# Kernel optimization log

Measured on AMD Instinct MI355X. Metric: run time of the kernel, lower is better.

## Reference

```python
import jax, jax.numpy as jnp
import numpy as np

C = 512          # channels
NH = 8           # num_heads
ENC = 512        # encoder_channels
SCALE_P = 1.0    # channels_scale_for_positional_embedding
CP = int(C * SCALE_P)
GROUPS = 32


def group_norm(x, g, b, eps=1e-5):
    # x: (N, C, L); GroupNorm32 computes stats in fp32
    N, Ch, L = x.shape
    xg = x.reshape(N, GROUPS, Ch // GROUPS, L).astype(jnp.float32)
    mu = xg.mean(axis=(2, 3), keepdims=True)
    var = xg.var(axis=(2, 3), keepdims=True)
    xn = ((xg - mu) * jax.lax.rsqrt(var + eps)).reshape(N, Ch, L).astype(x.dtype)
    return xn * g[None, :, None] + b[None, :, None]


def conv1(x, W, b):
    # 1x1 conv1d: x (N, Cin, L), W (Cout, Cin), b (Cout)
    return jnp.einsum('oc,ncl->nol', W, x) + b[None, :, None]


def setup_inputs() -> dict:
    key = jax.random.key(0)
    ks = iter(jax.random.split(key, 40))
    rn = lambda *s: jax.random.normal(next(ks), s, dtype=jnp.float32)
    inp = {
        'x': rn(8, C, 32, 32),
        'xf_out': rn(8, ENC, 64),
        'obj_contour_embedding': rn(8, ENC, 64),
        'obj_description_embedding': rn(8, ENC, 64),
        'image_patch_contour_embedding': rn(8, ENC, 1024),
        # norm_for_qkv
        'gn_qkv_g': jnp.ones(C), 'gn_qkv_b': jnp.zeros(C),
        # projectors (1x1 conv weights); zero_module proj_out given random weights for a meaningful baseline
        'W_self_qkv': rn(3 * C, C) * 0.02, 'b_self_qkv': jnp.zeros(3 * C),
        'W_cross_q': rn(C, C) * 0.02, 'b_cross_q': jnp.zeros(C),
        'W_content': rn(2 * C, ENC) * 0.02, 'b_content': jnp.zeros(2 * C),
        'W_pos': rn(CP, ENC) * 0.02, 'b_pos': jnp.zeros(CP),
        'gn_desc_g': jnp.ones(ENC), 'gn_desc_b': jnp.zeros(ENC),
        'gn_cpos_g': jnp.ones(CP), 'gn_cpos_b': jnp.zeros(CP),
        'gn_ipos_g': jnp.ones(CP), 'gn_ipos_b': jnp.zeros(CP),
        'W_self_out': rn(C, C) * 0.02, 'b_self_out': jnp.zeros(C),
        'W_cross_out': rn(C, C) * 0.02, 'b_cross_out': jnp.zeros(C),
    }
    return inp


def _attn(q, k, v, scale):
    # q,k: (B, Cq, T/S), v: (B, Cv, S)
    w = jnp.einsum('bct,bcs->bts', q * scale, k * scale)
    w = jax.nn.softmax(w.astype(jnp.float32), axis=-1).astype(q.dtype)
    return jnp.einsum('bts,bcs->bct', w, v)


def reference(x, xf_out, obj_contour_embedding, obj_description_embedding,
              image_patch_contour_embedding,
              gn_qkv_g, gn_qkv_b, W_self_qkv, b_self_qkv, W_cross_q, b_cross_q,
              W_content, b_content, W_pos, b_pos,
              gn_desc_g, gn_desc_b, gn_cpos_g, gn_cpos_b, gn_ipos_g, gn_ipos_b,
              W_self_out, b_self_out, W_cross_out, b_cross_out):
    b_, c_, h_, w_ = x.shape
    xf = x.reshape(b_, c_, -1)                      # (N, C, L1)
    L1 = xf.shape[-1]
    L2 = obj_contour_embedding.shape[-1]
    dc = C // NH
    dp = CP // NH
    scale = float(int((1 + SCALE_P) * C) // NH) ** -0.25

    # ---- self-attention over image patches ----
    qkv = conv1(group_norm(xf, gn_qkv_g, gn_qkv_b), W_self_qkv, b_self_qkv)
    sq, sk, sv = jnp.split(qkv, 3, axis=1)
    sq = sq.reshape(b_ * NH, dc, L1)
    sk = sk.reshape(b_ * NH, dc, L1)
    sv = sv.reshape(b_ * NH, dc, L1)

    ipos = conv1(image_patch_contour_embedding, W_pos, b_pos)
    ipos = group_norm(ipos, gn_ipos_g, gn_ipos_b)
    ipos = ipos.reshape(b_ * NH, dp, L1)

    sq = jnp.concatenate([sq, ipos], axis=1)
    sk = jnp.concatenate([sk, ipos], axis=1)
    self_out = _attn(sq, sk, sv, scale).reshape(b_, C, L1)
    self_out = conv1(self_out, W_self_out, b_self_out)
    xf = xf + self_out

    # ---- cross-attention to object tokens ----
    cq = conv1(group_norm(xf, gn_qkv_g, gn_qkv_b), W_cross_q, b_cross_q)
    cq = cq.reshape(b_ * NH, dc, L1)
    cq = jnp.concatenate([cq, ipos], axis=1)

    cpos = conv1(obj_contour_embedding, W_pos, b_pos)
    cpos = group_norm(cpos, gn_cpos_g, gn_cpos_b)
    cpos = cpos.reshape(b_ * NH, dp, L2)

    content = (xf_out + group_norm(obj_description_embedding, gn_desc_g, gn_desc_b)) / 2
    kv = conv1(content, W_content, b_content)
    ck, cv = jnp.split(kv, 2, axis=1)
    ck = ck.reshape(b_ * NH, dc, L2)
    cv = cv.reshape(b_ * NH, dc, L2)
    ck = jnp.concatenate([ck, cpos], axis=1)

    cross_out = _attn(cq, ck, cv, scale).reshape(b_, C, L1)
    cross_out = conv1(cross_out, W_cross_out, b_cross_out)

    return (xf + cross_out).reshape(b_, c_, h_, w_)
```

## Files before the change

kernel.cpp:

```cpp
#include <hip/hip_runtime.h>

typedef unsigned short u16;
typedef __attribute__((ext_vector_type(8))) short bf16x8;
typedef __attribute__((ext_vector_type(4))) float f32x4;

__device__ __forceinline__ float bf2f(u16 u) {
  union { unsigned int i; float f; } v;
  v.i = ((unsigned int)u) << 16;
  return v.f;
}
__device__ __forceinline__ u16 f2bf(float f) {
  union { float f; unsigned int i; } v;
  v.f = f;
  unsigned int r = v.i + 0x7FFFu + ((v.i >> 16) & 1u);
  return (u16)(r >> 16);
}
__device__ __forceinline__ unsigned int cvtpk(float lo, float hi) {
  unsigned int r;
  asm("v_cvt_pk_bf16_f32 %0, %1, %2" : "=v"(r) : "v"(lo), "v"(hi));
  return r;
}

__device__ __forceinline__ float4 ld4f(const float* p) {
  return *reinterpret_cast<const float4*>(p);
}
__device__ __forceinline__ float4 ld4f(const u16* p) {
  uint2 v = *reinterpret_cast<const uint2*>(p);
  float4 r;
  r.x = bf2f((u16)(v.x & 0xffff)); r.y = bf2f((u16)(v.x >> 16));
  r.z = bf2f((u16)(v.y & 0xffff)); r.w = bf2f((u16)(v.y >> 16));
  return r;
}

template <typename TIN>
__global__ __launch_bounds__(1024) void gn_kernel(
    const TIN* __restrict__ In, u16* __restrict__ OutBuf,
    const float* __restrict__ G, const float* __restrict__ Bt,
    const float* __restrict__ Add, float post_scale,
    int C, int L, int cpg)
{
  const int blk = blockIdx.x;
  const int n = blk >> 5, grp = blk & 31;
  const size_t base = ((size_t)n * C + (size_t)grp * cpg) * L;
  const int cnt = cpg * L;
  const int cnt4 = cnt >> 2;
  const int tid = threadIdx.x;

  float s = 0.f, s2 = 0.f;
  for (int i = tid; i < cnt4; i += 1024) {
    float4 v = ld4f(In + base + (size_t)i * 4);
    s += v.x + v.y + v.z + v.w;
    s2 += v.x * v.x + v.y * v.y + v.z * v.z + v.w * v.w;
  }
#pragma unroll
  for (int d = 1; d < 64; d <<= 1) {
    s += __shfl_xor(s, d);
    s2 += __shfl_xor(s2, d);
  }
  __shared__ float ps[16], ps2[16], stat[2];
  const int wid = tid >> 6;
  if ((tid & 63) == 0) { ps[wid] = s; ps2[wid] = s2; }
  __syncthreads();
  if (tid == 0) {
    float a = 0.f, b2 = 0.f;
#pragma unroll
    for (int w = 0; w < 16; ++w) { a += ps[w]; b2 += ps2[w]; }
    const float mean = a / cnt;
    const float var = b2 / cnt - mean * mean;
    stat[0] = mean;
    stat[1] = rsqrtf(var + 1e-5f);
  }
  __syncthreads();
  const float mean = stat[0], rstd = stat[1];

  for (int i = tid; i < cnt4; i += 1024) {
    const int i4 = i * 4;
    const int ch = grp * cpg + i4 / L;
    float4 v = ld4f(In + base + i4);
    const float g = G[ch] * rstd, bt = Bt[ch] - mean * rstd * G[ch];
    float4 r;
    r.x = v.x * g + bt; r.y = v.y * g + bt;
    r.z = v.z * g + bt; r.w = v.w * g + bt;
    if (Add) {
      float4 a = *reinterpret_cast<const float4*>(Add + base + i4);
      r.x = (r.x + a.x) * post_scale; r.y = (r.y + a.y) * post_scale;
      r.z = (r.z + a.z) * post_scale; r.w = (r.w + a.w) * post_scale;
    }
    uint2 o;
    o.x = (unsigned int)f2bf(r.x) | ((unsigned int)f2bf(r.y) << 16);
    o.y = (unsigned int)f2bf(r.z) | ((unsigned int)f2bf(r.w) << 16);
    *reinterpret_cast<uint2*>(OutBuf + base + i4) = o;
  }
}

__device__ __forceinline__ void loadpair4(const u16* p0, const u16* p1,
                                          unsigned int* bw) {
  uint2 a = *reinterpret_cast<const uint2*>(p0);
  uint2 c = *reinterpret_cast<const uint2*>(p1);
  bw[0] = (a.x & 0xffffu) | (c.x << 16);
  bw[1] = (a.x >> 16) | (c.x & 0xffff0000u);
  bw[2] = (a.y & 0xffffu) | (c.y << 16);
  bw[3] = (a.y >> 16) | (c.y & 0xffff0000u);
}
__device__ __forceinline__ void loadpair4(const float* p0, const float* p1,
                                          unsigned int* bw) {
  float4 a = *reinterpret_cast<const float4*>(p0);
  float4 c = *reinterpret_cast<const float4*>(p1);
  bw[0] = cvtpk(a.x, c.x); bw[1] = cvtpk(a.y, c.y);
  bw[2] = cvtpk(a.z, c.z); bw[3] = cvtpk(a.w, c.w);
}

template <typename TX, int LT>
__global__ __launch_bounds__(256) void gemm_conv(
    const TX* __restrict__ X, const float* __restrict__ W,
    const float* __restrict__ Bias,
    u16* __restrict__ OutBf, float* __restrict__ Out32,
    const float* __restrict__ Res,
    int Cin, int L, int O, int mode)
{
  constexpr int NL = LT / 16;
  __shared__ __align__(16) u16 As[64][40];
  __shared__ __align__(16) u16 Bs[LT][40];
  const int tid = threadIdx.x;
  const int wave = tid >> 6;
  const int lane = tid & 63;
  const int n = blockIdx.z;
  const int o0 = blockIdx.x * 64;
  const int l0 = blockIdx.y * LT;
  const TX* Xn = X + (size_t)n * Cin * L;

  const int ao = tid >> 2, akc = (tid & 3) * 8;
  const int c2 = (tid & 15) * 2, lt0 = (tid >> 4) * NL;
  const float* wp = W + (size_t)(o0 + ao) * Cin + akc;
  const TX* xp0 = Xn + (size_t)c2 * L + l0 + lt0;
  const TX* xp1 = xp0 + L;

  f32x4 acc[NL];
#pragma unroll
  for (int i = 0; i < NL; ++i) acc[i] = (f32x4){0.f, 0.f, 0.f, 0.f};

  const int row = lane & 15;
  const int kh = (lane >> 4) * 8;

  float4 wa = *reinterpret_cast<const float4*>(wp);
  float4 wb = *reinterpret_cast<const float4*>(wp + 4);
  unsigned int bw[NL];
#pragma unroll
  for (int ch = 0; ch < NL; ch += 4)
    loadpair4(xp0 + ch, xp1 + ch, bw + ch);

  const int nK = Cin >> 5;
  for (int kt = 0; kt < nK; ++kt) {
    {
      uint4 ap;
      ap.x = cvtpk(wa.x, wa.y); ap.y = cvtpk(wa.z, wa.w);
      ap.z = cvtpk(wb.x, wb.y); ap.w = cvtpk(wb.z, wb.w);
      *reinterpret_cast<uint4*>(&As[ao][akc]) = ap;
    }
#pragma unroll
    for (int j = 0; j < NL; ++j)
      *reinterpret_cast<unsigned int*>(&Bs[lt0 + j][c2]) = bw[j];
    __syncthreads();

    if (kt + 1 < nK) {
      const int k0 = (kt + 1) * 32;
      wa = *reinterpret_cast<const float4*>(wp + k0);
      wb = *reinterpret_cast<const float4*>(wp + k0 + 4);
#pragma unroll
      for (int ch = 0; ch < NL; ch += 4)
        loadpair4(xp0 + (size_t)k0 * L + ch, xp1 + (size_t)k0 * L + ch, bw + ch);
    }

    bf16x8 a = *reinterpret_cast<const bf16x8*>(&As[wave * 16 + row][kh]);
#pragma unroll
    for (int lt = 0; lt < NL; ++lt) {
      bf16x8 b = *reinterpret_cast<const bf16x8*>(&Bs[lt * 16 + row][kh]);
      acc[lt] = __builtin_amdgcn_mfma_f32_16x16x32_bf16(a, b, acc[lt], 0, 0, 0);
    }
    __syncthreads();
  }

  const int col = lane & 15;
  const int r0 = (lane >> 4) * 4;
#pragma unroll
  for (int lt = 0; lt < NL; ++lt) {
    const int ll = l0 + lt * 16 + col;
#pragma unroll
    for (int j = 0; j < 4; ++j) {
      const int oo = o0 + wave * 16 + r0 + j;
      float v = acc[lt][j] + Bias[oo];
      const size_t idx = ((size_t)n * O + oo) * L + ll;
      if (mode == 1) {
        Out32[idx] = v + Res[idx];
      } else {
        OutBf[idx] = f2bf(v);
      }
    }
  }
}

__global__ __launch_bounds__(256, 2) void flash_attn(
    const u16* __restrict__ qA, int qA_C, int qA_off,
    const u16* __restrict__ qB,
    const u16* __restrict__ kA, int kA_C, int kA_off,
    const u16* __restrict__ kB,
    const u16* __restrict__ V, int v_C, int v_off,
    u16* __restrict__ Out, int S_len, float qscale)
{
  __shared__ __align__(16) u16 smem[32768];
  u16* const Qs = smem;
  u16* const K0 = smem;
  u16* const K1 = smem + 8192;
  u16* const Ps = smem + 16384;
  u16* const V0 = smem + 24576;
  u16* const V1 = smem + 28672;

  const int tid = threadIdx.x;
  const int wave = tid >> 6, lane = tid & 63;
  const int b = blockIdx.y >> 3, h = blockIdx.y & 7;
  const int t0 = blockIdx.x * 128;
  const int l16 = lane & 15, q4 = lane >> 4;
  const int swz = (l16 & 7) << 3;

  const int c2 = (tid & 63) * 2;
  const u16* q0 = (c2 < 64)
      ? qA + ((size_t)b * qA_C + qA_off + h * 64 + c2) * 1024 + t0
      : qB + ((size_t)b * 512 + h * 64 + (c2 - 64)) * 1024 + t0;
  const u16* q1 = q0 + 1024;
  const u16* k0 = (c2 < 64)
      ? kA + ((size_t)b * kA_C + kA_off + h * 64 + c2) * (size_t)S_len
      : kB + ((size_t)b * 512 + h * 64 + (c2 - 64)) * (size_t)S_len;
  const u16* k1 = k0 + S_len;
  const u16* vb = V + ((size_t)b * v_C + v_off + h * 64) * (size_t)S_len;

  const int s8 = (tid >> 6) * 8;
  const int cv0 = tid >> 3, sb0 = (tid & 7) * 8;
  const int cv1 = (tid + 256) >> 3, sb1 = sb0;

  uint4 kr0a = *reinterpret_cast<const uint4*>(k0 + s8);
  uint4 kr0c = *reinterpret_cast<const uint4*>(k1 + s8);
  uint4 kr1a = *reinterpret_cast<const uint4*>(k0 + s8 + 32);
  uint4 kr1c = *reinterpret_cast<const uint4*>(k1 + s8 + 32);
  uint4 vr0 = *reinterpret_cast<const uint4*>(vb + (size_t)cv0 * S_len + sb0);
  uint4 vr1 = *reinterpret_cast<const uint4*>(vb + (size_t)cv1 * S_len + sb1);

#pragma unroll
  for (int it = 0; it < 4; ++it) {
    const int t8 = (tid >> 6) * 8 + it * 32;
    union { uint4 q; u16 u[8]; } a, c;
    a.q = *reinterpret_cast<const uint4*>(q0 + t8);
    c.q = *reinterpret_cast<const uint4*>(q1 + t8);
#pragma unroll
    for (int j = 0; j < 8; ++j) {
      const unsigned int w =
          cvtpk(bf2f(a.u[j]) * qscale, bf2f(c.u[j]) * qscale);
      *reinterpret_cast<unsigned int*>(&Qs[(t8 + j) * 128 + (c2 ^ (j << 3))]) = w;
    }
  }
  __syncthreads();

  bf16x8 qf[2][4];
#pragma unroll
  for (int g = 0; g < 2; ++g)
#pragma unroll
    for (int kk = 0; kk < 4; ++kk)
      qf[g][kk] = *reinterpret_cast<const bf16x8*>(
          &Qs[(wave * 32 + g * 16 + l16) * 128 + ((kk * 32 + q4 * 8) ^ swz)]);
  __syncthreads();

  auto writeK = [&](u16* Kd) {
    union { uint4 q; u16 u[8]; } a, c;
    a.q = kr0a; c.q = kr0c;
#pragma unroll
    for (int j = 0; j < 8; ++j)
      *reinterpret_cast<unsigned int*>(&Kd[(s8 + j) * 128 + (c2 ^ (j << 3))]) =
          (unsigned int)a.u[j] | ((unsigned int)c.u[j] << 16);
    a.q = kr1a; c.q = kr1c;
#pragma unroll
    for (int j = 0; j < 8; ++j)
      *reinterpret_cast<unsigned int*>(&Kd[(s8 + 32 + j) * 128 + (c2 ^ (j << 3))]) =
          (unsigned int)a.u[j] | ((unsigned int)c.u[j] << 16);
  };
  auto writeV = [&](u16* Vd) {
    *reinterpret_cast<uint4*>(&Vd[cv0 * 64 + (sb0 ^ ((cv0 & 7) << 3))]) = vr0;
    *reinterpret_cast<uint4*>(&Vd[cv1 * 64 + (sb1 ^ ((cv1 & 7) << 3))]) = vr1;
  };

  writeK(K0);
  writeV(V0);
  __syncthreads();

  float m_run[2][4], l_run[2][4];
  f32x4 o_acc[2][4];
#pragma unroll
  for (int g = 0; g < 2; ++g)
#pragma unroll
    for (int j = 0; j < 4; ++j) {
      m_run[g][j] = -1e30f; l_run[g][j] = 0.f;
      o_acc[g][j] = (f32x4){0.f, 0.f, 0.f, 0.f};
    }

  const int NT = S_len >> 6;
  int p = 0;
  for (int t = 0; t < NT; ++t) {
    u16* const Kp = p ? K1 : K0;
    u16* const Vp = p ? V1 : V0;

    if (t + 1 < NT) {
      const int sc = (t + 1) * 64;
      kr0a = *reinterpret_cast<const uint4*>(k0 + sc + s8);
      kr0c = *reinterpret_cast<const uint4*>(k1 + sc + s8);
      kr1a = *reinterpret_cast<const uint4*>(k0 + sc + s8 + 32);
      kr1c = *reinterpret_cast<const uint4*>(k1 + sc + s8 + 32);
      vr0 = *reinterpret_cast<const uint4*>(vb + (size_t)cv0 * S_len + sc + sb0);
      vr1 = *reinterpret_cast<const uint4*>(vb + (size_t)cv1 * S_len + sc + sb1);
    }

    f32x4 sacc[2][4];
#pragma unroll
    for (int g = 0; g < 2; ++g)
#pragma unroll
      for (int st = 0; st < 4; ++st) sacc[g][st] = (f32x4){0.f, 0.f, 0.f, 0.f};
    __builtin_amdgcn_s_setprio(1);
#pragma unroll
    for (int st = 0; st < 4; ++st) {
#pragma unroll
      for (int kk = 0; kk < 4; ++kk) {
        bf16x8 kf = *reinterpret_cast<const bf16x8*>(
            &Kp[(st * 16 + l16) * 128 + ((kk * 32 + q4 * 8) ^ swz)]);
        sacc[0][st] = __builtin_amdgcn_mfma_f32_16x16x32_bf16(qf[0][kk], kf, sacc[0][st], 0, 0, 0);
        sacc[1][st] = __builtin_amdgcn_mfma_f32_16x16x32_bf16(qf[1][kk], kf, sacc[1][st], 0, 0, 0);
      }
    }
    __builtin_amdgcn_s_setprio(0);

#pragma unroll
    for (int g = 0; g < 2; ++g) {
      float mt[4];
#pragma unroll
      for (int j = 0; j < 4; ++j)
        mt[j] = fmaxf(fmaxf(sacc[g][0][j], sacc[g][1][j]),
                      fmaxf(sacc[g][2][j], sacc[g][3][j]));
#pragma unroll
      for (int d = 1; d < 16; d <<= 1)
#pragma unroll
        for (int j = 0; j < 4; ++j) mt[j] = fmaxf(mt[j], __shfl_xor(mt[j], d));

      float corr[4], ls[4];
#pragma unroll
      for (int j = 0; j < 4; ++j) {
        const float mn = fmaxf(m_run[g][j], mt[j]);
        corr[j] = exp2f(m_run[g][j] - mn);
        m_run[g][j] = mn;
        ls[j] = 0.f;
      }
      float pv[4][4];
#pragma unroll
      for (int st = 0; st < 4; ++st)
#pragma unroll
        for (int j = 0; j < 4; ++j) {
          pv[st][j] = exp2f(sacc[g][st][j] - m_run[g][j]);
          ls[j] += pv[st][j];
        }
#pragma unroll
      for (int d = 1; d < 16; d <<= 1)
#pragma unroll
        for (int j = 0; j < 4; ++j) ls[j] += __shfl_xor(ls[j], d);
#pragma unroll
      for (int j = 0; j < 4; ++j) l_run[g][j] = l_run[g][j] * corr[j] + ls[j];

#pragma unroll
      for (int st = 0; st < 4; ++st)
#pragma unroll
        for (int j2 = 0; j2 < 2; ++j2) {
          const unsigned int pk = cvtpk(pv[st][2 * j2], pv[st][2 * j2 + 1]);
          const int r0 = wave * 32 + g * 16 + q4 * 4 + 2 * j2;
          Ps[r0 * 64 + ((st * 16 + l16) ^ ((r0 & 7) << 3))] = (u16)pk;
          const int r1 = r0 + 1;
          Ps[r1 * 64 + ((st * 16 + l16) ^ ((r1 & 7) << 3))] = (u16)(pk >> 16);
        }

#pragma unroll
      for (int ct = 0; ct < 4; ++ct)
#pragma unroll
        for (int j = 0; j < 4; ++j) o_acc[g][ct][j] *= corr[j];
    }

    bf16x8 pa[2][2];
#pragma unroll
    for (int g = 0; g < 2; ++g)
#pragma unroll
      for (int ks = 0; ks < 2; ++ks)
        pa[g][ks] = *reinterpret_cast<const bf16x8*>(
            &Ps[(wave * 32 + g * 16 + l16) * 64 + ((ks * 32 + q4 * 8) ^ swz)]);
    __builtin_amdgcn_s_setprio(1);
#pragma unroll
    for (int ct = 0; ct < 4; ++ct) {
#pragma unroll
      for (int ks = 0; ks < 2; ++ks) {
        bf16x8 vf = *reinterpret_cast<const bf16x8*>(
            &Vp[(ct * 16 + l16) * 64 + ((ks * 32 + q4 * 8) ^ swz)]);
        o_acc[0][ct] = __builtin_amdgcn_mfma_f32_16x16x32_bf16(pa[0][ks], vf, o_acc[0][ct], 0, 0, 0);
        o_acc[1][ct] = __builtin_amdgcn_mfma_f32_16x16x32_bf16(pa[1][ks], vf, o_acc[1][ct], 0, 0, 0);
      }
    }
    __builtin_amdgcn_s_setprio(0);

    if (t + 1 < NT) {
      writeK(p ? K0 : K1);
      writeV(p ? V0 : V1);
    }
    __syncthreads();
    p ^= 1;
  }

#pragma unroll
  for (int g = 0; g < 2; ++g) {
    float inv[4];
#pragma unroll
    for (int j = 0; j < 4; ++j) inv[j] = 1.f / l_run[g][j];
    const size_t obase =
        ((size_t)b * 512 + h * 64) * 1024 + t0 + wave * 32 + g * 16 + q4 * 4;
#pragma unroll
    for (int ct = 0; ct < 4; ++ct) {
      const unsigned int p0 = cvtpk(o_acc[g][ct][0] * inv[0], o_acc[g][ct][1] * inv[1]);
      const unsigned int p1 = cvtpk(o_acc[g][ct][2] * inv[2], o_acc[g][ct][3] * inv[3]);
      const unsigned long long d =
          (unsigned long long)p0 | ((unsigned long long)p1 << 32);
      *reinterpret_cast<unsigned long long*>(
          Out + obase + (size_t)(ct * 16 + l16) * 1024) = d;
    }
  }
}

extern "C" void kernel_launch(void* const* d_in, const int* in_sizes, int n_in,
                              void* d_out, int out_size, void* d_ws, size_t ws_size,
                              hipStream_t stream) {
  const float* X_in        = (const float*)d_in[0];
  const float* xf_out      = (const float*)d_in[1];
  const float* obj_cont    = (const float*)d_in[2];
  const float* obj_desc    = (const float*)d_in[3];
  const float* ipce        = (const float*)d_in[4];
  const float* gn_qkv_g    = (const float*)d_in[5];
  const float* gn_qkv_b    = (const float*)d_in[6];
  const float* W_self_qkv  = (const float*)d_in[7];
  const float* b_self_qkv  = (const float*)d_in[8];
  const float* W_cross_q   = (const float*)d_in[9];
  const float* b_cross_q   = (const float*)d_in[10];
  const float* W_content   = (const float*)d_in[11];
  const float* b_content   = (const float*)d_in[12];
  const float* W_pos       = (const float*)d_in[13];
  const float* b_pos       = (const float*)d_in[14];
  const float* gn_desc_g   = (const float*)d_in[15];
  const float* gn_desc_b   = (const float*)d_in[16];
  const float* gn_cpos_g   = (const float*)d_in[17];
  const float* gn_cpos_b   = (const float*)d_in[18];
  const float* gn_ipos_g   = (const float*)d_in[19];
  const float* gn_ipos_b   = (const float*)d_in[20];
  const float* W_self_out  = (const float*)d_in[21];
  const float* b_self_out  = (const float*)d_in[22];
  const float* W_cross_out = (const float*)d_in[23];
  const float* b_cross_out = (const float*)d_in[24];

  char* base = (char*)d_ws;
  u16* A = (u16*)base;
  u16* B = (u16*)(base + 8 * 1024 * 1024);
  u16* C = (u16*)(base + 32 * 1024 * 1024);
  u16* D = (u16*)(base + 40 * 1024 * 1024);

  u16* norm1 = A;
  u16* norm2 = A;
  u16* cposr   = A;
  u16* cpos    = A + 262144;
  u16* content = A + 2 * 262144;
  u16* kvbuf   = A + 3 * 262144;
  u16* qkv  = B;
  u16* cq   = B;
  u16* ipos = C;
  u16* iposr = D;
  u16* attn1 = D;
  u16* cattn = D;
  float* xf32 = (float*)d_out;
  float* outp = (float*)d_out;

  const float qscale = 0.08838834764831845f * 1.4426950408889634f;
  dim3 blk(256);
  dim3 blkgn(1024);

  gn_kernel<float><<<dim3(256), blkgn, 0, stream>>>(X_in, norm1, gn_qkv_g, gn_qkv_b,
                                                    nullptr, 1.f, 512, 1024, 16);
  gemm_conv<u16, 128><<<dim3(24, 8, 8), blk, 0, stream>>>(norm1, W_self_qkv, b_self_qkv,
                                                          qkv, nullptr, nullptr,
                                                          512, 1024, 1536, 0);
  gemm_conv<float, 128><<<dim3(8, 8, 8), blk, 0, stream>>>(ipce, W_pos, b_pos, iposr,
                                                           nullptr, nullptr,
                                                           512, 1024, 512, 0);
  gn_kernel<u16><<<dim3(256), blkgn, 0, stream>>>(iposr, ipos, gn_ipos_g, gn_ipos_b,
                                                  nullptr, 1.f, 512, 1024, 16);
  flash_attn<<<dim3(8, 64), blk, 0, stream>>>(qkv, 1536, 0, ipos,
                                              qkv, 1536, 512, ipos,
                                              qkv, 1536, 1024,
                                              attn1, 1024, qscale);
  gemm_conv<u16, 128><<<dim3(8, 8, 8), blk, 0, stream>>>(attn1, W_self_out, b_self_out,
                                                         nullptr, xf32, X_in,
                                                         512, 1024, 512, 1);
  gn_kernel<float><<<dim3(256), blkgn, 0, stream>>>(xf32, norm2, gn_qkv_g, gn_qkv_b,
                                                    nullptr, 1.f, 512, 1024, 16);
  gemm_conv<u16, 128><<<dim3(8, 8, 8), blk, 0, stream>>>(norm2, W_cross_q, b_cross_q, cq,
                                                         nullptr, nullptr,
                                                         512, 1024, 512, 0);
  gemm_conv<float, 64><<<dim3(8, 1, 8), blk, 0, stream>>>(obj_cont, W_pos, b_pos, cposr,
                                                          nullptr, nullptr,
                                                          512, 64, 512, 0);
  gn_kernel<u16><<<dim3(256), blkgn, 0, stream>>>(cposr, cpos, gn_cpos_g, gn_cpos_b,
                                                  nullptr, 1.f, 512, 64, 16);
  gn_kernel<float><<<dim3(256), blkgn, 0, stream>>>(obj_desc, content, gn_desc_g,
                                                    gn_desc_b, xf_out, 0.5f, 512, 64, 16);
  gemm_conv<u16, 64><<<dim3(16, 1, 8), blk, 0, stream>>>(content, W_content, b_content,
                                                         kvbuf, nullptr, nullptr,
                                                         512, 64, 1024, 0);
  flash_attn<<<dim3(8, 64), blk, 0, stream>>>(cq, 512, 0, ipos,
                                              kvbuf, 1024, 0, cpos,
                                              kvbuf, 1024, 512,
                                              cattn, 64, qscale);
  gemm_conv<u16, 128><<<dim3(8, 8, 8), blk, 0, stream>>>(cattn, W_cross_out, b_cross_out,
                                                         nullptr, outp, xf32,
                                                         512, 1024, 512, 1);
}
```

Measured before the change: 295.8 us.

## Use 128x128 GEMM tiles with 512 threads and single-buffer attention K/V

The large 1x1-conv GEMMs move from 64x128 tiles with 256 threads to 128x128 tiles with 512 threads (8 waves), so each block covers more output channels and reuses each staged input tile more. Small-L GEMMs get their own 64x64 kernel. Flash attention drops K/V double buffering to a single LDS buffer that is written at the top of each iteration, which cuts shared memory use but serialises loads against compute. The P and output packing also switch from v_cvt_pk_bf16 to per-element software rounding.

```diff
diff --git a/kernel.cpp b/kernel.cpp
--- a/kernel.cpp
+++ b/kernel.cpp
@@ -110,44 +110,40 @@
   bw[2] = cvtpk(a.z, c.z); bw[3] = cvtpk(a.w, c.w);
 }
 
-template <typename TX, int LT>
-__global__ __launch_bounds__(256) void gemm_conv(
+template <typename TX>
+__global__ __launch_bounds__(256) void gemm_small(
     const TX* __restrict__ X, const float* __restrict__ W,
     const float* __restrict__ Bias,
-    u16* __restrict__ OutBf, float* __restrict__ Out32,
-    const float* __restrict__ Res,
-    int Cin, int L, int O, int mode)
+    u16* __restrict__ OutBf,
+    int Cin, int L, int O)
 {
-  constexpr int NL = LT / 16;
   __shared__ __align__(16) u16 As[64][40];
-  __shared__ __align__(16) u16 Bs[LT][40];
+  __shared__ __align__(16) u16 Bs[64][40];
   const int tid = threadIdx.x;
   const int wave = tid >> 6;
   const int lane = tid & 63;
   const int n = blockIdx.z;
   const int o0 = blockIdx.x * 64;
-  const int l0 = blockIdx.y * LT;
+  const int l0 = blockIdx.y * 64;
   const TX* Xn = X + (size_t)n * Cin * L;
 
   const int ao = tid >> 2, akc = (tid & 3) * 8;
-  const int c2 = (tid & 15) * 2, lt0 = (tid >> 4) * NL;
+  const int c2 = (tid & 15) * 2, lt0 = (tid >> 4) * 4;
   const float* wp = W + (size_t)(o0 + ao) * Cin + akc;
   const TX* xp0 = Xn + (size_t)c2 * L + l0 + lt0;
   const TX* xp1 = xp0 + L;
 
-  f32x4 acc[NL];
-#pragma unroll
-  for (int i = 0; i < NL; ++i) acc[i] = (f32x4){0.f, 0.f, 0.f, 0.f};
+  f32x4 acc[4];
+#pragma unroll
+  for (int i = 0; i < 4; ++i) acc[i] = (f32x4){0.f, 0.f, 0.f, 0.f};
 
   const int row = lane & 15;
   const int kh = (lane >> 4) * 8;
 
   float4 wa = *reinterpret_cast<const float4*>(wp);
   float4 wb = *reinterpret_cast<const float4*>(wp + 4);
-  unsigned int bw[NL];
-#pragma unroll
-  for (int ch = 0; ch < NL; ch += 4)
-    loadpair4(xp0 + ch, xp1 + ch, bw + ch);
+  unsigned int bw[4];
+  loadpair4(xp0, xp1, bw);
 
   const int nK = Cin >> 5;
   for (int kt = 0; kt < nK; ++kt) {
@@ -158,7 +154,7 @@
       *reinterpret_cast<uint4*>(&As[ao][akc]) = ap;
     }
 #pragma unroll
-    for (int j = 0; j < NL; ++j)
+    for (int j = 0; j < 4; ++j)
       *reinterpret_cast<unsigned int*>(&Bs[lt0 + j][c2]) = bw[j];
     __syncthreads();
 
@@ -166,14 +162,12 @@
       const int k0 = (kt + 1) * 32;
       wa = *reinterpret_cast<const float4*>(wp + k0);
       wb = *reinterpret_cast<const float4*>(wp + k0 + 4);
-#pragma unroll
-      for (int ch = 0; ch < NL; ch += 4)
-        loadpair4(xp0 + (size_t)k0 * L + ch, xp1 + (size_t)k0 * L + ch, bw + ch);
+      loadpair4(xp0 + (size_t)k0 * L, xp1 + (size_t)k0 * L, bw);
     }
 
     bf16x8 a = *reinterpret_cast<const bf16x8*>(&As[wave * 16 + row][kh]);
 #pragma unroll
-    for (int lt = 0; lt < NL; ++lt) {
+    for (int lt = 0; lt < 4; ++lt) {
       bf16x8 b = *reinterpret_cast<const bf16x8*>(&Bs[lt * 16 + row][kh]);
       acc[lt] = __builtin_amdgcn_mfma_f32_16x16x32_bf16(a, b, acc[lt], 0, 0, 0);
     }
@@ -183,7 +177,86 @@
   const int col = lane & 15;
   const int r0 = (lane >> 4) * 4;
 #pragma unroll
-  for (int lt = 0; lt < NL; ++lt) {
+  for (int lt = 0; lt < 4; ++lt) {
+    const int ll = l0 + lt * 16 + col;
+#pragma unroll
+    for (int j = 0; j < 4; ++j) {
+      const int oo = o0 + wave * 16 + r0 + j;
+      float v = acc[lt][j] + Bias[oo];
+      OutBf[((size_t)n * O + oo) * L + ll] = f2bf(v);
+    }
+  }
+}
+
+template <typename TX>
+__global__ __launch_bounds__(512) void gemm_big(
+    const TX* __restrict__ X, const float* __restrict__ W,
+    const float* __restrict__ Bias,
+    u16* __restrict__ OutBf, float* __restrict__ Out32,
+    const float* __restrict__ Res,
+    int Cin, int L, int O, int mode)
+{
+  __shared__ __align__(16) u16 As[128][40];
+  __shared__ __align__(16) u16 Bs[128][40];
+  const int tid = threadIdx.x;
+  const int wave = tid >> 6;
+  const int lane = tid & 63;
+  const int n = blockIdx.z;
+  const int o0 = blockIdx.x * 128;
+  const int l0 = blockIdx.y * 128;
+  const TX* Xn = X + (size_t)n * Cin * L;
+
+  const int ao = tid >> 2, akc = (tid & 3) * 8;
+  const int c2 = (tid & 15) * 2, lt0 = (tid >> 4) * 4;
+  const float* wp = W + (size_t)(o0 + ao) * Cin + akc;
+  const TX* xp0 = Xn + (size_t)c2 * L + l0 + lt0;
+  const TX* xp1 = xp0 + L;
+
+  f32x4 acc[8];
+#pragma unroll
+  for (int i = 0; i < 8; ++i) acc[i] = (f32x4){0.f, 0.f, 0.f, 0.f};
+
+  const int row = lane & 15;
+  const int kh = (lane >> 4) * 8;
+
+  float4 wa = *reinterpret_cast<const float4*>(wp);
+  float4 wb = *reinterpret_cast<const float4*>(wp + 4);
+  unsigned int bw[4];
+  loadpair4(xp0, xp1, bw);
+
+  const int nK = Cin >> 5;
+  for (int kt = 0; kt < nK; ++kt) {
+    {
+      uint4 ap;
+      ap.x = cvtpk(wa.x, wa.y); ap.y = cvtpk(wa.z, wa.w);
+      ap.z = cvtpk(wb.x, wb.y); ap.w = cvtpk(wb.z, wb.w);
+      *reinterpret_cast<uint4*>(&As[ao][akc]) = ap;
+    }
+#pragma unroll
+    for (int j = 0; j < 4; ++j)
+      *reinterpret_cast<unsigned int*>(&Bs[lt0 + j][c2]) = bw[j];
+    __syncthreads();
+
+    if (kt + 1 < nK) {
+      const int k0 = (kt + 1) * 32;
+      wa = *reinterpret_cast<const float4*>(wp + k0);
+      wb = *reinterpret_cast<const float4*>(wp + k0 + 4);
+      loadpair4(xp0 + (size_t)k0 * L, xp1 + (size_t)k0 * L, bw);
+    }
+
+    bf16x8 a = *reinterpret_cast<const bf16x8*>(&As[wave * 16 + row][kh]);
+#pragma unroll
+    for (int lt = 0; lt < 8; ++lt) {
+      bf16x8 b = *reinterpret_cast<const bf16x8*>(&Bs[lt * 16 + row][kh]);
+      acc[lt] = __builtin_amdgcn_mfma_f32_16x16x32_bf16(a, b, acc[lt], 0, 0, 0);
+    }
+    __syncthreads();
+  }
+
+  const int col = lane & 15;
+  const int r0 = (lane >> 4) * 4;
+#pragma unroll
+  for (int lt = 0; lt < 8; ++lt) {
     const int ll = l0 + lt * 16 + col;
 #pragma unroll
     for (int j = 0; j < 4; ++j) {
@@ -207,13 +280,11 @@
     const u16* __restrict__ V, int v_C, int v_off,
     u16* __restrict__ Out, int S_len, float qscale)
 {
-  __shared__ __align__(16) u16 smem[32768];
+  __shared__ __align__(16) u16 smem[20480];
   u16* const Qs = smem;
-  u16* const K0 = smem;
-  u16* const K1 = smem + 8192;
-  u16* const Ps = smem + 16384;
-  u16* const V0 = smem + 24576;
-  u16* const V1 = smem + 28672;
+  u16* const Ks = smem;
+  u16* const Ps = smem + 8192;
+  u16* const Vt = smem + 16384;
 
   const int tid = threadIdx.x;
   const int wave = tid >> 6, lane = tid & 63;
@@ -268,28 +339,6 @@
           &Qs[(wave * 32 + g * 16 + l16) * 128 + ((kk * 32 + q4 * 8) ^ swz)]);
   __syncthreads();
 
-  auto writeK = [&](u16* Kd) {
-    union { uint4 q; u16 u[8]; } a, c;
-    a.q = kr0a; c.q = kr0c;
-#pragma unroll
-    for (int j = 0; j < 8; ++j)
-      *reinterpret_cast<unsigned int*>(&Kd[(s8 + j) * 128 + (c2 ^ (j << 3))]) =
-          (unsigned int)a.u[j] | ((unsigned int)c.u[j] << 16);
-    a.q = kr1a; c.q = kr1c;
-#pragma unroll
-    for (int j = 0; j < 8; ++j)
-      *reinterpret_cast<unsigned int*>(&Kd[(s8 + 32 + j) * 128 + (c2 ^ (j << 3))]) =
-          (unsigned int)a.u[j] | ((unsigned int)c.u[j] << 16);
-  };
-  auto writeV = [&](u16* Vd) {
-    *reinterpret_cast<uint4*>(&Vd[cv0 * 64 + (sb0 ^ ((cv0 & 7) << 3))]) = vr0;
-    *reinterpret_cast<uint4*>(&Vd[cv1 * 64 + (sb1 ^ ((cv1 & 7) << 3))]) = vr1;
-  };
-
-  writeK(K0);
-  writeV(V0);
-  __syncthreads();
-
   float m_run[2][4], l_run[2][4];
   f32x4 o_acc[2][4];
 #pragma unroll
@@ -301,10 +350,23 @@
     }
 
   const int NT = S_len >> 6;
-  int p = 0;
   for (int t = 0; t < NT; ++t) {
-    u16* const Kp = p ? K1 : K0;
-    u16* const Vp = p ? V1 : V0;
+    {
+      union { uint4 q; u16 u[8]; } a, c;
+      a.q = kr0a; c.q = kr0c;
+#pragma unroll
+      for (int j = 0; j < 8; ++j)
+        *reinterpret_cast<unsigned int*>(&Ks[(s8 + j) * 128 + (c2 ^ (j << 3))]) =
+            (unsigned int)a.u[j] | ((unsigned int)c.u[j] << 16);
+      a.q = kr1a; c.q = kr1c;
+#pragma unroll
+      for (int j = 0; j < 8; ++j)
+        *reinterpret_cast<unsigned int*>(&Ks[(s8 + 32 + j) * 128 + (c2 ^ (j << 3))]) =
+            (unsigned int)a.u[j] | ((unsigned int)c.u[j] << 16);
+    }
+    *reinterpret_cast<uint4*>(&Vt[cv0 * 64 + (sb0 ^ ((cv0 & 7) << 3))]) = vr0;
+    *reinterpret_cast<uint4*>(&Vt[cv1 * 64 + (sb1 ^ ((cv1 & 7) << 3))]) = vr1;
+    __syncthreads();
 
     if (t + 1 < NT) {
       const int sc = (t + 1) * 64;
@@ -327,7 +389,7 @@
 #pragma unroll
       for (int kk = 0; kk < 4; ++kk) {
         bf16x8 kf = *reinterpret_cast<const bf16x8*>(
-            &Kp[(st * 16 + l16) * 128 + ((kk * 32 + q4 * 8) ^ swz)]);
+            &Ks[(st * 16 + l16) * 128 + ((kk * 32 + q4 * 8) ^ swz)]);
         sacc[0][st] = __builtin_amdgcn_mfma_f32_16x16x32_bf16(qf[0][kk], kf, sacc[0][st], 0, 0, 0);
         sacc[1][st] = __builtin_amdgcn_mfma_f32_16x16x32_bf16(qf[1][kk], kf, sacc[1][st], 0, 0, 0);
       }
@@ -372,13 +434,9 @@
 #pragma unroll
       for (int st = 0; st < 4; ++st)
 #pragma unroll
-        for (int j2 = 0; j2 < 2; ++j2) {
-          const unsigned int pk = cvtpk(pv[st][2 * j2], pv[st][2 * j2 + 1]);
-          const int r0 = wave * 32 + g * 16 + q4 * 4 + 2 * j2;
-          Ps[r0 * 64 + ((st * 16 + l16) ^ ((r0 & 7) << 3))] = (u16)pk;
-          const int r1 = r0 + 1;
-          Ps[r1 * 64 + ((st * 16 + l16) ^ ((r1 & 7) << 3))] = (u16)(pk >> 16);
-        }
+        for (int j = 0; j < 4; ++j)
+          Ps[(wave * 32 + g * 16 + q4 * 4 + j) * 64 +
+             ((st * 16 + l16) ^ (((q4 * 4 + j) & 7) << 3))] = f2bf(pv[st][j]);
 
 #pragma unroll
       for (int ct = 0; ct < 4; ++ct)
@@ -399,19 +457,13 @@
 #pragma unroll
       for (int ks = 0; ks < 2; ++ks) {
         bf16x8 vf = *reinterpret_cast<const bf16x8*>(
-            &Vp[(ct * 16 + l16) * 64 + ((ks * 32 + q4 * 8) ^ swz)]);
+            &Vt[(ct * 16 + l16) * 64 + ((ks * 32 + q4 * 8) ^ swz)]);
         o_acc[0][ct] = __builtin_amdgcn_mfma_f32_16x16x32_bf16(pa[0][ks], vf, o_acc[0][ct], 0, 0, 0);
         o_acc[1][ct] = __builtin_amdgcn_mfma_f32_16x16x32_bf16(pa[1][ks], vf, o_acc[1][ct], 0, 0, 0);
       }
     }
     __builtin_amdgcn_s_setprio(0);
-
-    if (t + 1 < NT) {
-      writeK(p ? K0 : K1);
-      writeV(p ? V0 : V1);
-    }
     __syncthreads();
-    p ^= 1;
   }
 
 #pragma unroll
@@ -423,12 +475,11 @@
         ((size_t)b * 512 + h * 64) * 1024 + t0 + wave * 32 + g * 16 + q4 * 4;
 #pragma unroll
     for (int ct = 0; ct < 4; ++ct) {
-      const unsigned int p0 = cvtpk(o_acc[g][ct][0] * inv[0], o_acc[g][ct][1] * inv[1]);
-      const unsigned int p1 = cvtpk(o_acc[g][ct][2] * inv[2], o_acc[g][ct][3] * inv[3]);
-      const unsigned long long d =
-          (unsigned long long)p0 | ((unsigned long long)p1 << 32);
+      union { unsigned long long d; u16 u[4]; } pk;
+#pragma unroll
+      for (int j = 0; j < 4; ++j) pk.u[j] = f2bf(o_acc[g][ct][j] * inv[j]);
       *reinterpret_cast<unsigned long long*>(
-          Out + obase + (size_t)(ct * 16 + l16) * 1024) = d;
+          Out + obase + (size_t)(ct * 16 + l16) * 1024) = pk.d;
     }
   }
 }
@@ -485,45 +536,44 @@
 
   const float qscale = 0.08838834764831845f * 1.4426950408889634f;
   dim3 blk(256);
+  dim3 blkg(512);
   dim3 blkgn(1024);
 
   gn_kernel<float><<<dim3(256), blkgn, 0, stream>>>(X_in, norm1, gn_qkv_g, gn_qkv_b,
                                                     nullptr, 1.f, 512, 1024, 16);
-  gemm_conv<u16, 128><<<dim3(24, 8, 8), blk, 0, stream>>>(norm1, W_self_qkv, b_self_qkv,
-                                                          qkv, nullptr, nullptr,
-                                                          512, 1024, 1536, 0);
-  gemm_conv<float, 128><<<dim3(8, 8, 8), blk, 0, stream>>>(ipce, W_pos, b_pos, iposr,
-                                                           nullptr, nullptr,
-                                                           512, 1024, 512, 0);
+  gemm_big<u16><<<dim3(12, 8, 8), blkg, 0, stream>>>(norm1, W_self_qkv, b_self_qkv,
+                                                     qkv, nullptr, nullptr,
+                                                     512, 1024, 1536, 0);
+  gemm_big<float><<<dim3(4, 8, 8), blkg, 0, stream>>>(ipce, W_pos, b_pos, iposr,
+                                                      nullptr, nullptr,
+                                                      512, 1024, 512, 0);
   gn_kernel<u16><<<dim3(256), blkgn, 0, stream>>>(iposr, ipos, gn_ipos_g, gn_ipos_b,
                                                   nullptr, 1.f, 512, 1024, 16);
   flash_attn<<<dim3(8, 64), blk, 0, stream>>>(qkv, 1536, 0, ipos,
                                               qkv, 1536, 512, ipos,
                                               qkv, 1536, 1024,
                                               attn1, 1024, qscale);
-  gemm_conv<u16, 128><<<dim3(8, 8, 8), blk, 0, stream>>>(attn1, W_self_out, b_self_out,
-                                                         nullptr, xf32, X_in,
-                                                         512, 1024, 512, 1);
+  gemm_big<u16><<<dim3(4, 8, 8), blkg, 0, stream>>>(attn1, W_self_out, b_self_out,
+                                                    nullptr, xf32, X_in,
+                                                    512, 1024, 512, 1);
   gn_kernel<float><<<dim3(256), blkgn, 0, stream>>>(xf32, norm2, gn_qkv_g, gn_qkv_b,
                                                     nullptr, 1.f, 512, 1024, 16);
-  gemm_conv<u16, 128><<<dim3(8, 8, 8), blk, 0, stream>>>(norm2, W_cross_q, b_cross_q, cq,
-                                                         nullptr, nullptr,
-                                                         512, 1024, 512, 0);
-  gemm_conv<float, 64><<<dim3(8, 1, 8), blk, 0, stream>>>(obj_cont, W_pos, b_pos, cposr,
-                                                          nullptr, nullptr,
-                                                          512, 64, 512, 0);
+  gemm_big<u16><<<dim3(4, 8, 8), blkg, 0, stream>>>(norm2, W_cross_q, b_cross_q, cq,
+                                                    nullptr, nullptr,
+                                                    512, 1024, 512, 0);
+  gemm_small<float><<<dim3(8, 1, 8), blk, 0, stream>>>(obj_cont, W_pos, b_pos, cposr,
+                                                       512, 64, 512);
   gn_kernel<u16><<<dim3(256), blkgn, 0, stream>>>(cposr, cpos, gn_cpos_g, gn_cpos_b,
                                                   nullptr, 1.f, 512, 64, 16);
   gn_kernel<float><<<dim3(256), blkgn, 0, stream>>>(obj_desc, content, gn_desc_g,
                                                     gn_desc_b, xf_out, 0.5f, 512, 64, 16);
-  gemm_conv<u16, 64><<<dim3(16, 1, 8), blk, 0, stream>>>(content, W_content, b_content,
-                                                         kvbuf, nullptr, nullptr,
-                                                         512, 64, 1024, 0);
+  gemm_small<u16><<<dim3(16, 1, 8), blk, 0, stream>>>(content, W_content, b_content,
+                                                      kvbuf, 512, 64, 1024);
   flash_attn<<<dim3(8, 64), blk, 0, stream>>>(cq, 512, 0, ipos,
                                               kvbuf, 1024, 0, cpos,
                                               kvbuf, 1024, 512,
                                               cattn, 64, qscale);
-  gemm_conv<u16, 128><<<dim3(8, 8, 8), blk, 0, stream>>>(cattn, W_cross_out, b_cross_out,
-                                                         nullptr, outp, xf32,
-                                                         512, 1024, 512, 1);
-}
+  gemm_big<u16><<<dim3(4, 8, 8), blkg, 0, stream>>>(cattn, W_cross_out, b_cross_out,
+                                                    nullptr, outp, xf32,
+                                                    512, 1024, 512, 1);
+}
```

New measurement: 288.8 us. 2.3% less time.
